# Performance work log

Measured on AMD Instinct MI355X. Metric: run time of the kernel, lower is better.

## Reference

```python
import jax, jax.numpy as jnp
import numpy as np

EMB = 1024
HID = 1024
VOCAB = 32000
SEQ = 128


def _lstm_cell(x, h, c, W_ih, W_hh, b_ih, b_hh):
    # PyTorch gate order: input, forget, cell(g), output
    gates = x @ W_ih.T + b_ih + h @ W_hh.T + b_hh  # [4H]
    i, f, g, o = jnp.split(gates, 4)
    c_new = jax.nn.sigmoid(f) * c + jax.nn.sigmoid(i) * jnp.tanh(g)
    h_new = jax.nn.sigmoid(o) * jnp.tanh(c_new)
    return h_new, c_new


def setup_inputs() -> dict:
    key = jax.random.key(0)
    ks = jax.random.split(key, 12)
    s_emb = 0.02
    s_lstm = 1.0 / np.sqrt(HID)
    return {
        "sentence": jax.random.randint(ks[0], (SEQ,), 0, VOCAB),
        "given_num": 64,
        "emb": jax.random.normal(ks[1], (VOCAB, EMB), jnp.float32) * s_emb,
        "W_ih_lstm": jax.random.normal(ks[2], (4 * HID, EMB), jnp.float32) * s_lstm,
        "W_hh_lstm": jax.random.normal(ks[3], (4 * HID, HID), jnp.float32) * s_lstm,
        "b_ih_lstm": jax.random.normal(ks[4], (4 * HID,), jnp.float32) * s_lstm,
        "b_hh_lstm": jax.random.normal(ks[5], (4 * HID,), jnp.float32) * s_lstm,
        "W_ih_cell": jax.random.normal(ks[6], (4 * HID, EMB), jnp.float32) * s_lstm,
        "W_hh_cell": jax.random.normal(ks[7], (4 * HID, HID), jnp.float32) * s_lstm,
        "b_ih_cell": jax.random.normal(ks[8], (4 * HID,), jnp.float32) * s_lstm,
        "b_hh_cell": jax.random.normal(ks[9], (4 * HID,), jnp.float32) * s_lstm,
        "W_tag": jax.random.normal(ks[10], (VOCAB, HID), jnp.float32) * s_lstm,
        "b_tag": jax.random.normal(ks[11], (VOCAB,), jnp.float32) * s_lstm,
    }


def reference(sentence, given_num, emb, W_ih_lstm, W_hh_lstm, b_ih_lstm, b_hh_lstm,
              W_ih_cell, W_hh_cell, b_ih_cell, b_hh_cell, W_tag, b_tag):
    given_num = int(given_num)  # static (batch-1 rollout, fixed split point)

    # ---- teacher-forced prefix through nn.LSTM (init_hidden -> zeros) ----
    embeds_existing = emb[sentence[:given_num]]  # [g, E]

    def prefix_step(carry, x):
        h, c = carry
        h, c = _lstm_cell(x, h, c, W_ih_lstm, W_hh_lstm, b_ih_lstm, b_hh_lstm)
        return (h, c), h

    h0 = jnp.zeros((HID,), embeds_existing.dtype)
    (h, c), lstm_out = jax.lax.scan(prefix_step, (h0, h0), embeds_existing)
    tag_prefix = lstm_out @ W_tag.T + b_tag  # [g, V]

    # multinomial over softmax(tag) == categorical over logits; only last row's
    # sample is consumed as x_t
    skeys = jax.random.split(jax.random.key(123), SEQ - given_num + 1)
    x_t = jax.random.categorical(skeys[0], tag_prefix[-1])

    def rollout_step(carry, k):
        x_t, h, c = carry
        e = emb[x_t]
        h, c = _lstm_cell(e, h, c, W_ih_cell, W_hh_cell, b_ih_cell, b_hh_cell)
        logits = h @ W_tag.T + b_tag  # [V]
        x_next = jax.random.categorical(k, logits)
        return (x_next, h, c), logits

    _, tag_roll = jax.lax.scan(rollout_step, (x_t, h, c), skeys[1:])  # [S-g, V]

    tag_space = jnp.concatenate([tag_prefix, tag_roll], axis=0)  # [S, V]
    return jax.nn.log_softmax(tag_space, axis=-1)
```

## Files before the change

kernel.cpp:

```cpp
#include <hip/hip_runtime.h>
#include <hip/hip_fp16.h>
#include <cstdint>
#include <cstddef>

#define EMBD 1024
#define HIDD 1024
#define G4   4096
#define VOC  32000
#define SEQL 128
#define GN   64
#define NR   64

#define JAX_PARTITIONABLE 1

__device__ __forceinline__ uint32_t rotl32(uint32_t v, int d) { return (v << d) | (v >> (32 - d)); }

__device__ inline void threefry2x32(uint32_t k0, uint32_t k1, uint32_t x0, uint32_t x1,
                                    uint32_t& o0, uint32_t& o1) {
  uint32_t ks2 = k0 ^ k1 ^ 0x1BD11BDAu;
#define TF_ROUND(r) { x0 += x1; x1 = rotl32(x1, r); x1 ^= x0; }
  x0 += k0;  x1 += k1;
  TF_ROUND(13) TF_ROUND(15) TF_ROUND(26) TF_ROUND(6)
  x0 += k1;  x1 += ks2 + 1u;
  TF_ROUND(17) TF_ROUND(29) TF_ROUND(16) TF_ROUND(24)
  x0 += ks2; x1 += k0 + 2u;
  TF_ROUND(13) TF_ROUND(15) TF_ROUND(26) TF_ROUND(6)
  x0 += k0;  x1 += k1 + 3u;
  TF_ROUND(17) TF_ROUND(29) TF_ROUND(16) TF_ROUND(24)
  x0 += k1;  x1 += ks2 + 4u;
  TF_ROUND(13) TF_ROUND(15) TF_ROUND(26) TF_ROUND(6)
  x0 += ks2; x1 += k0 + 5u;
#undef TF_ROUND
  o0 = x0; o1 = x1;
}

__device__ inline uint32_t rng_bits(uint32_t k0, uint32_t k1, uint32_t idx) {
#if JAX_PARTITIONABLE
  uint32_t h0, h1; threefry2x32(k0, k1, 0u, idx, h0, h1);
  return h0 ^ h1;
#else
  uint32_t h0, h1;
  if (idx < (VOC / 2)) { threefry2x32(k0, k1, idx, idx + (VOC / 2), h0, h1); return h0; }
  else                 { threefry2x32(k0, k1, idx - (VOC / 2), idx, h0, h1); return h1; }
#endif
}

__device__ inline float gumbel_of(uint32_t k0, uint32_t k1, uint32_t idx) {
  uint32_t bits = rng_bits(k0, k1, idx);
  float u = __uint_as_float((bits >> 9) | 0x3f800000u) - 1.0f;
  u = fmaxf(u, 1.17549435e-38f);
  return -logf(-logf(u));
}

__device__ inline unsigned long long packCand(float v, int idx) {
  uint32_t u = __float_as_uint(v);
  u = (u & 0x80000000u) ? ~u : (u | 0x80000000u);
  return ((unsigned long long)u << 32) | (unsigned long long)(0xFFFFFFFFu - (uint32_t)idx);
}

__device__ inline float sigf(float x) { return 1.0f / (1.0f + expf(-x)); }

__device__ __forceinline__ float h2f(unsigned short u) {
  __half_raw hr; hr.x = u;
  return __half2float(__half(hr));
}

__global__ void k_init(uint2* keys, unsigned* counters, float* cbuf, float* h0) {
  int t = threadIdx.x;
#if JAX_PARTITIONABLE
  if (t < NR + 1) {
    uint32_t a, b; threefry2x32(0u, 123u, 0u, (uint32_t)t, a, b);
    keys[t] = make_uint2(a, b);
  }
#else
  __shared__ uint32_t buf[2 * (NR + 1)];
  if (t < NR + 1) {
    uint32_t a, b; threefry2x32(0u, 123u, (uint32_t)t, (uint32_t)(t + NR + 1), a, b);
    buf[t] = a; buf[t + NR + 1] = b;
  }
  __syncthreads();
  if (t < NR + 1) keys[t] = make_uint2(buf[2 * t], buf[2 * t + 1]);
#endif
  for (int i = t; i < 66; i += 256) counters[i] = 0u;
  for (int i = t; i < HIDD; i += 256) { cbuf[i] = 0.0f; h0[i] = 0.0f; }
}

__global__ __launch_bounds__(256) void k_cvt_f16(const float* __restrict__ src,
                                                 unsigned short* __restrict__ dst, int n) {
  int stride = gridDim.x * blockDim.x * 8;
  for (int i = (blockIdx.x * blockDim.x + threadIdx.x) * 8; i < n; i += stride) {
    float4 a = *(const float4*)(src + i);
    float4 b = *(const float4*)(src + i + 4);
    union { unsigned short u[8]; uint4 v; } p;
    __half t;
    t = __float2half(a.x); p.u[0] = __half_raw(t).x;
    t = __float2half(a.y); p.u[1] = __half_raw(t).x;
    t = __float2half(a.z); p.u[2] = __half_raw(t).x;
    t = __float2half(a.w); p.u[3] = __half_raw(t).x;
    t = __float2half(b.x); p.u[4] = __half_raw(t).x;
    t = __float2half(b.y); p.u[5] = __half_raw(t).x;
    t = __float2half(b.z); p.u[6] = __half_raw(t).x;
    t = __float2half(b.w); p.u[7] = __half_raw(t).x;
    *(uint4*)(dst + i) = p.v;
  }
}

__global__ void k_gather(const float* __restrict__ emb, const int* __restrict__ sent,
                         float* __restrict__ X) {
  int m = blockIdx.x;
  int row = sent[m];
  const float4* s = (const float4*)(emb + (size_t)row * EMBD);
  float4* d = (float4*)(X + (size_t)m * EMBD);
  d[threadIdx.x] = s[threadIdx.x];
}

__global__ __launch_bounds__(256) void k_gemm64(const float* __restrict__ A,
                                                const float* __restrict__ B,
                                                const float* __restrict__ bias,
                                                float* __restrict__ C, int ldc) {
  __shared__ float As[64][33];
  __shared__ float Bs[64][33];
  int n0 = blockIdx.x * 64;
  int tn = threadIdx.x & 15, tm = threadIdx.x >> 4;
  float acc[4][4] = {{0.f}};
  for (int k0 = 0; k0 < 1024; k0 += 32) {
    for (int f = threadIdx.x; f < 512; f += 256) {
      int r = f >> 3, c4 = (f & 7) << 2;
      float4 v = *(const float4*)(A + (size_t)r * 1024 + k0 + c4);
      As[r][c4 + 0] = v.x; As[r][c4 + 1] = v.y; As[r][c4 + 2] = v.z; As[r][c4 + 3] = v.w;
      float4 u = *(const float4*)(B + (size_t)(n0 + r) * 1024 + k0 + c4);
      Bs[r][c4 + 0] = u.x; Bs[r][c4 + 1] = u.y; Bs[r][c4 + 2] = u.z; Bs[r][c4 + 3] = u.w;
    }
    __syncthreads();
#pragma unroll
    for (int kk = 0; kk < 32; ++kk) {
      float a0 = As[tm * 4 + 0][kk], a1 = As[tm * 4 + 1][kk];
      float a2 = As[tm * 4 + 2][kk], a3 = As[tm * 4 + 3][kk];
      float b0 = Bs[tn * 4 + 0][kk], b1 = Bs[tn * 4 + 1][kk];
      float b2 = Bs[tn * 4 + 2][kk], b3 = Bs[tn * 4 + 3][kk];
      acc[0][0] += a0 * b0; acc[0][1] += a0 * b1; acc[0][2] += a0 * b2; acc[0][3] += a0 * b3;
      acc[1][0] += a1 * b0; acc[1][1] += a1 * b1; acc[1][2] += a1 * b2; acc[1][3] += a1 * b3;
      acc[2][0] += a2 * b0; acc[2][1] += a2 * b1; acc[2][2] += a2 * b2; acc[2][3] += a2 * b3;
      acc[3][0] += a3 * b0; acc[3][1] += a3 * b1; acc[3][2] += a3 * b2; acc[3][3] += a3 * b3;
    }
    __syncthreads();
  }
#pragma unroll
  for (int i = 0; i < 4; ++i)
#pragma unroll
    for (int j = 0; j < 4; ++j) {
      int m = tm * 4 + i, n = n0 + tn * 4 + j;
      float r = acc[i][j] + (bias ? bias[n] : 0.0f);
      C[(size_t)m * ldc + n] = r;
    }
}

__global__ __launch_bounds__(256) void k_gemm64_f16b(const float* __restrict__ A,
                                                     const unsigned short* __restrict__ B16,
                                                     const float* __restrict__ bias,
                                                     float* __restrict__ C, int ldc) {
  __shared__ float As[64][33];
  __shared__ float Bs[64][33];
  int n0 = blockIdx.x * 64;
  int tn = threadIdx.x & 15, tm = threadIdx.x >> 4;
  float acc[4][4] = {{0.f}};
  for (int k0 = 0; k0 < 1024; k0 += 32) {
    for (int f = threadIdx.x; f < 512; f += 256) {
      int r = f >> 3, c4 = (f & 7) << 2;
      float4 v = *(const float4*)(A + (size_t)r * 1024 + k0 + c4);
      As[r][c4 + 0] = v.x; As[r][c4 + 1] = v.y; As[r][c4 + 2] = v.z; As[r][c4 + 3] = v.w;
    }
    {
      int f = threadIdx.x;
      int r = f >> 2, c8 = (f & 3) << 3;
      union { uint4 v; unsigned short u[8]; } p;
      p.v = *(const uint4*)(B16 + (size_t)(n0 + r) * 1024 + k0 + c8);
#pragma unroll
      for (int j = 0; j < 8; ++j) Bs[r][c8 + j] = h2f(p.u[j]);
    }
    __syncthreads();
#pragma unroll
    for (int kk = 0; kk < 32; ++kk) {
      float a0 = As[tm * 4 + 0][kk], a1 = As[tm * 4 + 1][kk];
      float a2 = As[tm * 4 + 2][kk], a3 = As[tm * 4 + 3][kk];
      float b0 = Bs[tn * 4 + 0][kk], b1 = Bs[tn * 4 + 1][kk];
      float b2 = Bs[tn * 4 + 2][kk], b3 = Bs[tn * 4 + 3][kk];
      acc[0][0] += a0 * b0; acc[0][1] += a0 * b1; acc[0][2] += a0 * b2; acc[0][3] += a0 * b3;
      acc[1][0] += a1 * b0; acc[1][1] += a1 * b1; acc[1][2] += a1 * b2; acc[1][3] += a1 * b3;
      acc[2][0] += a2 * b0; acc[2][1] += a2 * b1; acc[2][2] += a2 * b2; acc[2][3] += a2 * b3;
      acc[3][0] += a3 * b0; acc[3][1] += a3 * b1; acc[3][2] += a3 * b2; acc[3][3] += a3 * b3;
    }
    __syncthreads();
  }
#pragma unroll
  for (int i = 0; i < 4; ++i)
#pragma unroll
    for (int j = 0; j < 4; ++j) {
      int m = tm * 4 + i, n = n0 + tn * 4 + j;
      float r = acc[i][j] + (bias ? bias[n] : 0.0f);
      C[(size_t)m * ldc + n] = r;
    }
}

__global__ __launch_bounds__(256) void k_lstm_pre(const float* __restrict__ Whh,
                                                  const float* __restrict__ bih,
                                                  const float* __restrict__ bhh,
                                                  const float* __restrict__ gx, int t,
                                                  const float* __restrict__ hprev,
                                                  float* __restrict__ cbuf,
                                                  float* __restrict__ hout) {
  __shared__ float gs[4];
  int wave = threadIdx.x >> 6, lane = threadIdx.x & 63;
  int j = blockIdx.x;
  int r = j + (wave << 10);
  const float4* h4 = (const float4*)hprev;
  const float4* w4 = (const float4*)(Whh + (size_t)r * 1024);
  float a = 0.0f;
#pragma unroll
  for (int q = 0; q < 4; ++q) {
    float4 w = w4[lane + (q << 6)];
    float4 h = h4[lane + (q << 6)];
    a += w.x * h.x + w.y * h.y + w.z * h.z + w.w * h.w;
  }
#pragma unroll
  for (int off = 32; off; off >>= 1) a += __shfl_xor(a, off, 64);
  if (lane == 0) gs[wave] = a + gx[(size_t)t * G4 + r] + bih[r] + bhh[r];
  __syncthreads();
  if (threadIdx.x == 0) {
    float gi = gs[0], gf = gs[1], gg = gs[2], go = gs[3];
    float cn = sigf(gf) * cbuf[j] + sigf(gi) * tanhf(gg);
    cbuf[j] = cn;
    hout[j] = sigf(go) * tanhf(cn);
  }
}

__global__ __launch_bounds__(256) void k_lstm_roll(const float* __restrict__ Wih,
                                                   const float* __restrict__ Whh,
                                                   const float* __restrict__ bih,
                                                   const float* __restrict__ bhh,
                                                   const float* __restrict__ emb,
                                                   const int* __restrict__ tok, int t,
                                                   const float* __restrict__ hprev,
                                                   float* __restrict__ cbuf,
                                                   float* __restrict__ hout) {
  __shared__ float gs[4];
  int wave = threadIdx.x >> 6, lane = threadIdx.x & 63;
  int j = blockIdx.x;
  int r = j + (wave << 10);
  int row = tok[t];
  const float4* x4 = (const float4*)(emb + (size_t)row * EMBD);
  const float4* h4 = (const float4*)hprev;
  const float4* wi = (const float4*)(Wih + (size_t)r * 1024);
  const float4* wh = (const float4*)(Whh + (size_t)r * 1024);
  float a = 0.0f;
#pragma unroll
  for (int q = 0; q < 4; ++q) {
    float4 w = wi[lane + (q << 6)];
    float4 x = x4[lane + (q << 6)];
    a += w.x * x.x + w.y * x.y + w.z * x.z + w.w * x.w;
    w = wh[lane + (q << 6)];
    float4 h = h4[lane + (q << 6)];
    a += w.x * h.x + w.y * h.y + w.z * h.z + w.w * h.w;
  }
#pragma unroll
  for (int off = 32; off; off >>= 1) a += __shfl_xor(a, off, 64);
  if (lane == 0) gs[wave] = a + bih[r] + bhh[r];
  __syncthreads();
  if (threadIdx.x == 0) {
    float gi = gs[0], gf = gs[1], gg = gs[2], go = gs[3];
    float cn = sigf(gf) * cbuf[j] + sigf(gi) * tanhf(gg);
    cbuf[j] = cn;
    hout[j] = sigf(go) * tanhf(cn);
  }
}

__global__ __launch_bounds__(256) void k_logits(const float* __restrict__ Wtag,
                                                const float* __restrict__ btag,
                                                const float* __restrict__ h,
                                                float* __restrict__ outrow,
                                                const uint2* __restrict__ keys, int key_idx,
                                                unsigned long long* __restrict__ partials,
                                                unsigned* __restrict__ counter,
                                                int* __restrict__ token_out) {
  __shared__ float sums[64];
  __shared__ unsigned long long red[256];
  __shared__ int amLast;
  int wave = threadIdx.x >> 6, lane = threadIdx.x & 63;
  int r0 = blockIdx.x * 64;
  const float4* h4 = (const float4*)h;
  float4 hv[4];
#pragma unroll
  for (int q = 0; q < 4; ++q) hv[q] = h4[lane + (q << 6)];
  for (int rr = 0; rr < 16; ++rr) {
    int lr = wave * 16 + rr;
    int r = r0 + lr;
    const float4* w4 = (const float4*)(Wtag + (size_t)r * 1024);
    float a = 0.0f;
#pragma unroll
    for (int q = 0; q < 4; ++q) {
      float4 w = w4[lane + (q << 6)];
      a += w.x * hv[q].x + w.y * hv[q].y + w.z * hv[q].z + w.w * hv[q].w;
    }
#pragma unroll
    for (int off = 32; off; off >>= 1) a += __shfl_xor(a, off, 64);
    if (lane == 0) sums[lr] = a;
  }
  __syncthreads();
  unsigned long long best = 0ull;
  if (threadIdx.x < 64) {
    int r = r0 + threadIdx.x;
    float L = sums[threadIdx.x] + btag[r];
    outrow[r] = L;
    uint2 K = keys[key_idx];
    float y = L + gumbel_of(K.x, K.y, (uint32_t)r);
    best = packCand(y, r);
#pragma unroll
    for (int off = 32; off; off >>= 1) {
      unsigned long long o = __shfl_xor(best, off, 64);
      if (o > best) best = o;
    }
    if (threadIdx.x == 0) partials[blockIdx.x] = best;
  }
  __threadfence();
  __syncthreads();
  if (threadIdx.x == 0) amLast = (atomicAdd(counter, 1u) == gridDim.x - 1) ? 1 : 0;
  __syncthreads();
  if (amLast) {
    __threadfence();
    unsigned long long b = 0ull;
    for (int i = threadIdx.x; i < (int)gridDim.x; i += 256) {
      unsigned long long v = *((volatile unsigned long long*)(partials + i));
      if (v > b) b = v;
    }
    red[threadIdx.x] = b;
    __syncthreads();
    for (int s = 128; s; s >>= 1) {
      if (threadIdx.x < s) {
        if (red[threadIdx.x + s] > red[threadIdx.x]) red[threadIdx.x] = red[threadIdx.x + s];
      }
      __syncthreads();
    }
    if (threadIdx.x == 0)
      token_out[0] = (int)(0xFFFFFFFFu - (uint32_t)(red[0] & 0xFFFFFFFFull));
  }
}

__global__ __launch_bounds__(256) void k_logits_f16(const unsigned short* __restrict__ Wt16,
                                                    const float* __restrict__ btag,
                                                    const float* __restrict__ h,
                                                    float* __restrict__ outrow,
                                                    const uint2* __restrict__ keys, int key_idx,
                                                    unsigned long long* __restrict__ partials,
                                                    unsigned* __restrict__ counter,
                                                    int* __restrict__ token_out) {
  __shared__ float sums[64];
  __shared__ unsigned long long red[256];
  __shared__ int amLast;
  int wave = threadIdx.x >> 6, lane = threadIdx.x & 63;
  int r0 = blockIdx.x * 64;
  const float4* h4 = (const float4*)h;
  float4 hq[4];
#pragma unroll
  for (int q = 0; q < 2; ++q) {
    hq[2 * q]     = h4[q * 128 + lane * 2];
    hq[2 * q + 1] = h4[q * 128 + lane * 2 + 1];
  }
  for (int rr = 0; rr < 16; ++rr) {
    int lr = wave * 16 + rr;
    int r = r0 + lr;
    const unsigned short* wrow = Wt16 + (size_t)r * 1024;
    float a = 0.0f;
#pragma unroll
    for (int q = 0; q < 2; ++q) {
      union { uint4 v; unsigned short u[8]; } p;
      p.v = *(const uint4*)(wrow + q * 512 + lane * 8);
      float4 hA = hq[2 * q], hB = hq[2 * q + 1];
      a += h2f(p.u[0]) * hA.x; a += h2f(p.u[1]) * hA.y;
      a += h2f(p.u[2]) * hA.z; a += h2f(p.u[3]) * hA.w;
      a += h2f(p.u[4]) * hB.x; a += h2f(p.u[5]) * hB.y;
      a += h2f(p.u[6]) * hB.z; a += h2f(p.u[7]) * hB.w;
    }
#pragma unroll
    for (int off = 32; off; off >>= 1) a += __shfl_xor(a, off, 64);
    if (lane == 0) sums[lr] = a;
  }
  __syncthreads();
  unsigned long long best = 0ull;
  if (threadIdx.x < 64) {
    int r = r0 + threadIdx.x;
    float L = sums[threadIdx.x] + btag[r];
    outrow[r] = L;
    uint2 K = keys[key_idx];
    float y = L + gumbel_of(K.x, K.y, (uint32_t)r);
    best = packCand(y, r);
#pragma unroll
    for (int off = 32; off; off >>= 1) {
      unsigned long long o = __shfl_xor(best, off, 64);
      if (o > best) best = o;
    }
    if (threadIdx.x == 0) partials[blockIdx.x] = best;
  }
  __threadfence();
  __syncthreads();
  if (threadIdx.x == 0) amLast = (atomicAdd(counter, 1u) == gridDim.x - 1) ? 1 : 0;
  __syncthreads();
  if (amLast) {
    __threadfence();
    unsigned long long b = 0ull;
    for (int i = threadIdx.x; i < (int)gridDim.x; i += 256) {
      unsigned long long v = *((volatile unsigned long long*)(partials + i));
      if (v > b) b = v;
    }
    red[threadIdx.x] = b;
    __syncthreads();
    for (int s = 128; s; s >>= 1) {
      if (threadIdx.x < s) {
        if (red[threadIdx.x + s] > red[threadIdx.x]) red[threadIdx.x] = red[threadIdx.x + s];
      }
      __syncthreads();
    }
    if (threadIdx.x == 0)
      token_out[0] = (int)(0xFFFFFFFFu - (uint32_t)(red[0] & 0xFFFFFFFFull));
  }
}

__global__ __launch_bounds__(256) void k_sample_row(const float* __restrict__ row,
                                                    const uint2* __restrict__ keys, int key_idx,
                                                    unsigned long long* __restrict__ partials,
                                                    unsigned* __restrict__ counter,
                                                    int* __restrict__ token_out) {
  __shared__ unsigned long long red[256];
  __shared__ int amLast;
  int v = blockIdx.x * 256 + threadIdx.x;
  unsigned long long best = 0ull;
  if (v < VOC) {
    uint2 K = keys[key_idx];
    float y = row[v] + gumbel_of(K.x, K.y, (uint32_t)v);
    best = packCand(y, v);
  }
  red[threadIdx.x] = best;
  __syncthreads();
  for (int s = 128; s; s >>= 1) {
    if (threadIdx.x < s) {
      if (red[threadIdx.x + s] > red[threadIdx.x]) red[threadIdx.x] = red[threadIdx.x + s];
    }
    __syncthreads();
  }
  if (threadIdx.x == 0) partials[blockIdx.x] = red[0];
  __threadfence();
  __syncthreads();
  if (threadIdx.x == 0) amLast = (atomicAdd(counter, 1u) == gridDim.x - 1) ? 1 : 0;
  __syncthreads();
  if (amLast) {
    __threadfence();
    unsigned long long b = 0ull;
    for (int i = threadIdx.x; i < (int)gridDim.x; i += 256) {
      unsigned long long val = *((volatile unsigned long long*)(partials + i));
      if (val > b) b = val;
    }
    red[threadIdx.x] = b;
    __syncthreads();
    for (int s = 128; s; s >>= 1) {
      if (threadIdx.x < s) {
        if (red[threadIdx.x + s] > red[threadIdx.x]) red[threadIdx.x] = red[threadIdx.x + s];
      }
      __syncthreads();
    }
    if (threadIdx.x == 0)
      token_out[0] = (int)(0xFFFFFFFFu - (uint32_t)(red[0] & 0xFFFFFFFFull));
  }
}

__global__ __launch_bounds__(256) void k_logsoftmax(float* __restrict__ C) {
  __shared__ float red[256];
  float* row = C + (size_t)blockIdx.x * VOC;
  float m = -INFINITY;
  for (int i = threadIdx.x; i < VOC; i += 256) m = fmaxf(m, row[i]);
  red[threadIdx.x] = m;
  __syncthreads();
  for (int s = 128; s; s >>= 1) {
    if (threadIdx.x < s) red[threadIdx.x] = fmaxf(red[threadIdx.x], red[threadIdx.x + s]);
    __syncthreads();
  }
  m = red[0];
  __syncthreads();
  float sum = 0.0f;
  for (int i = threadIdx.x; i < VOC; i += 256) sum += expf(row[i] - m);
  red[threadIdx.x] = sum;
  __syncthreads();
  for (int s = 128; s; s >>= 1) {
    if (threadIdx.x < s) red[threadIdx.x] += red[threadIdx.x + s];
    __syncthreads();
  }
  float lse = m + logf(red[0]);
  __syncthreads();
  for (int i = threadIdx.x; i < VOC; i += 256) row[i] = row[i] - lse;
}

extern "C" void kernel_launch(void* const* d_in, const int* in_sizes, int n_in,
                              void* d_out, int out_size, void* d_ws, size_t ws_size,
                              hipStream_t stream) {
  (void)in_sizes; (void)n_in; (void)out_size;
  const int*   sent  = (const int*)  d_in[0];
  const float* emb   = (const float*)d_in[2];
  const float* Wih_l = (const float*)d_in[3];
  const float* Whh_l = (const float*)d_in[4];
  const float* bih_l = (const float*)d_in[5];
  const float* bhh_l = (const float*)d_in[6];
  const float* Wih_c = (const float*)d_in[7];
  const float* Whh_c = (const float*)d_in[8];
  const float* bih_c = (const float*)d_in[9];
  const float* bhh_c = (const float*)d_in[10];
  const float* Wtag  = (const float*)d_in[11];
  const float* btag  = (const float*)d_in[12];
  float* out = (float*)d_out;

  char* ws = (char*)d_ws;
  uint2*              keys     = (uint2*)(ws + 0);
  int*                tokens   = (int*)(ws + 1024);
  unsigned*           counters = (unsigned*)(ws + 2048);
  unsigned long long* partials = (unsigned long long*)(ws + 4096);
  float*              cbuf     = (float*)(ws + 12288);
  float*              h0       = (float*)(ws + 16384);
  float*              lstm_out = (float*)(ws + 20480);
  float*              hroll    = (float*)(ws + 20480 + 262144);
  float*              X        = (float*)(ws + 20480 + 2 * 262144);
  float*              gx       = (float*)(ws + 20480 + 3 * 262144);
  const size_t WT16_OFF   = 2u * 1024u * 1024u;
  const size_t WT16_BYTES = (size_t)VOC * 1024u * 2u;
  unsigned short* Wt16 = (unsigned short*)(ws + WT16_OFF);
  bool use16 = (ws_size >= WT16_OFF + WT16_BYTES);

  k_init<<<1, 256, 0, stream>>>(keys, counters, cbuf, h0);
  if (use16)
    k_cvt_f16<<<2048, 256, 0, stream>>>(Wtag, Wt16, VOC * 1024);
  k_gather<<<GN, 256, 0, stream>>>(emb, sent, X);
  k_gemm64<<<G4 / 64, 256, 0, stream>>>(X, Wih_l, nullptr, gx, G4);
  for (int t = 0; t < GN; ++t) {
    const float* hp = t ? (lstm_out + (size_t)(t - 1) * HIDD) : h0;
    k_lstm_pre<<<HIDD, 256, 0, stream>>>(Whh_l, bih_l, bhh_l, gx, t, hp, cbuf,
                                         lstm_out + (size_t)t * HIDD);
  }
  if (use16)
    k_gemm64_f16b<<<VOC / 64, 256, 0, stream>>>(lstm_out, Wt16, btag, out, VOC);
  else
    k_gemm64<<<VOC / 64, 256, 0, stream>>>(lstm_out, Wtag, btag, out, VOC);
  k_sample_row<<<(VOC + 255) / 256, 256, 0, stream>>>(out + (size_t)(GN - 1) * VOC, keys, 0,
                                                      partials, counters + 64, tokens);
  for (int t = 0; t < NR; ++t) {
    const float* hp = t ? (hroll + (size_t)(t - 1) * HIDD) : (lstm_out + (size_t)(GN - 1) * HIDD);
    k_lstm_roll<<<HIDD, 256, 0, stream>>>(Wih_c, Whh_c, bih_c, bhh_c, emb, tokens, t, hp, cbuf,
                                          hroll + (size_t)t * HIDD);
    if (use16)
      k_logits_f16<<<VOC / 64, 256, 0, stream>>>(Wt16, btag, hroll + (size_t)t * HIDD,
                                                 out + (size_t)(GN + t) * VOC, keys, 1 + t,
                                                 partials, counters + t, tokens + t + 1);
    else
      k_logits<<<VOC / 64, 256, 0, stream>>>(Wtag, btag, hroll + (size_t)t * HIDD,
                                             out + (size_t)(GN + t) * VOC, keys, 1 + t,
                                             partials, counters + t, tokens + t + 1);
  }
  k_logsoftmax<<<SEQL, 256, 0, stream>>>(out);
}
```

Before: 4.464 ms.

## Replace per-step LSTM launches with persistent kernels using grid barriers

Result: slower. 5.063 ms (+13.4%).

```diff
diff --git a/kernel.cpp b/kernel.cpp
--- a/kernel.cpp
+++ b/kernel.cpp
@@ -65,7 +65,21 @@
   return __half2float(__half(hr));
 }
 
-__global__ void k_init(uint2* keys, unsigned* counters, float* cbuf, float* h0) {
+__device__ __forceinline__ void gbar(unsigned* bar, unsigned target) {
+  __syncthreads();
+  if (threadIdx.x == 0) {
+    __threadfence();
+    unsigned prev = atomicAdd(bar, 1u);
+    if (prev + 1u < target) {
+      while (*((volatile unsigned*)bar) < target) __builtin_amdgcn_s_sleep(2);
+    }
+    __threadfence();
+  }
+  __syncthreads();
+}
+
+__global__ void k_init(uint2* keys, unsigned* counters, unsigned* bars,
+                       float* cbuf, float* h0) {
   int t = threadIdx.x;
 #if JAX_PARTITIONABLE
   if (t < NR + 1) {
@@ -82,6 +96,7 @@
   if (t < NR + 1) keys[t] = make_uint2(buf[2 * t], buf[2 * t + 1]);
 #endif
   for (int i = t; i < 66; i += 256) counters[i] = 0u;
+  for (int i = t; i < 1024; i += 256) bars[i] = 0u;
   for (int i = t; i < HIDD; i += 256) { cbuf[i] = 0.0f; h0[i] = 0.0f; }
 }
 
@@ -200,6 +215,167 @@
       float r = acc[i][j] + (bias ? bias[n] : 0.0f);
       C[(size_t)m * ldc + n] = r;
     }
+}
+
+__global__ __launch_bounds__(512) void k_prefix_persist(
+    const float* __restrict__ Whh, const float* __restrict__ bih,
+    const float* __restrict__ bhh, const float* __restrict__ gx,
+    const float* __restrict__ h0, float* __restrict__ lstm_out,
+    float* __restrict__ cbuf_out, unsigned* __restrict__ bars) {
+  int b = blockIdx.x;
+  int wave = threadIdx.x >> 6, lane = threadIdx.x & 63;
+  int j0 = b * 4;
+  __shared__ float gs[16];
+  __shared__ float cl[4];
+  if (threadIdx.x < 4) cl[threadIdx.x] = 0.0f;
+  __syncthreads();
+  for (int t = 0; t < GN; ++t) {
+    const float* hprev = t ? (lstm_out + (size_t)(t - 1) * HIDD) : h0;
+    const float4* h4 = (const float4*)hprev;
+    float4 hv[4];
+#pragma unroll
+    for (int q = 0; q < 4; ++q) hv[q] = h4[lane + (q << 6)];
+#pragma unroll
+    for (int rr = 0; rr < 2; ++rr) {
+      int rl = wave + (rr << 3);
+      int gate = rl >> 2, jj = rl & 3;
+      int r = (j0 + jj) + (gate << 10);
+      const float4* w4 = (const float4*)(Whh + (size_t)r * 1024);
+      float a = 0.0f;
+#pragma unroll
+      for (int q = 0; q < 4; ++q) {
+        float4 w = w4[lane + (q << 6)];
+        a += w.x * hv[q].x + w.y * hv[q].y + w.z * hv[q].z + w.w * hv[q].w;
+      }
+#pragma unroll
+      for (int off = 32; off; off >>= 1) a += __shfl_xor(a, off, 64);
+      if (lane == 0) gs[rl] = a + gx[(size_t)t * G4 + r] + bih[r] + bhh[r];
+    }
+    __syncthreads();
+    if (threadIdx.x < 4) {
+      int jj = threadIdx.x;
+      float gi = gs[jj], gf = gs[4 + jj], gg = gs[8 + jj], go = gs[12 + jj];
+      float cn = sigf(gf) * cl[jj] + sigf(gi) * tanhf(gg);
+      cl[jj] = cn;
+      lstm_out[(size_t)t * HIDD + j0 + jj] = sigf(go) * tanhf(cn);
+      if (t == GN - 1) cbuf_out[j0 + jj] = cn;
+    }
+    gbar(bars + t, gridDim.x);
+  }
+}
+
+__global__ __launch_bounds__(512) void k_roll_persist(
+    const float* __restrict__ Wih, const float* __restrict__ Whh,
+    const float* __restrict__ bih, const float* __restrict__ bhh,
+    const float* __restrict__ emb, const unsigned short* __restrict__ Wt16,
+    const float* __restrict__ btag, const float* __restrict__ cbuf_in,
+    const float* __restrict__ h_last, float* __restrict__ hbuf,
+    float* __restrict__ out, const uint2* __restrict__ keys,
+    int* __restrict__ tokens, unsigned long long* __restrict__ partials,
+    unsigned* __restrict__ bars) {
+  int b = blockIdx.x;
+  int wave = threadIdx.x >> 6, lane = threadIdx.x & 63;
+  int j0 = b * 4;
+  __shared__ float gs[16];
+  __shared__ float cl[4];
+  __shared__ unsigned long long wmax[8];
+  __shared__ unsigned long long pr[256];
+  if (threadIdx.x < 4) cl[threadIdx.x] = cbuf_in[j0 + threadIdx.x];
+  int token = tokens[0];
+  __syncthreads();
+  for (int t = 0; t < NR; ++t) {
+    const float* hprev = t ? (hbuf + (size_t)(t - 1) * HIDD) : h_last;
+    const float4* h4 = (const float4*)hprev;
+    const float4* x4 = (const float4*)(emb + (size_t)token * EMBD);
+    float4 hv[4], xv[4];
+#pragma unroll
+    for (int q = 0; q < 4; ++q) { hv[q] = h4[lane + (q << 6)]; xv[q] = x4[lane + (q << 6)]; }
+#pragma unroll
+    for (int rr = 0; rr < 2; ++rr) {
+      int rl = wave + (rr << 3);
+      int gate = rl >> 2, jj = rl & 3;
+      int r = (j0 + jj) + (gate << 10);
+      const float4* wi = (const float4*)(Wih + (size_t)r * 1024);
+      const float4* wh = (const float4*)(Whh + (size_t)r * 1024);
+      float a = 0.0f;
+#pragma unroll
+      for (int q = 0; q < 4; ++q) {
+        float4 w = wi[lane + (q << 6)];
+        a += w.x * xv[q].x + w.y * xv[q].y + w.z * xv[q].z + w.w * xv[q].w;
+        w = wh[lane + (q << 6)];
+        a += w.x * hv[q].x + w.y * hv[q].y + w.z * hv[q].z + w.w * hv[q].w;
+      }
+#pragma unroll
+      for (int off = 32; off; off >>= 1) a += __shfl_xor(a, off, 64);
+      if (lane == 0) gs[rl] = a + bih[r] + bhh[r];
+    }
+    __syncthreads();
+    if (threadIdx.x < 4) {
+      int jj = threadIdx.x;
+      float gi = gs[jj], gf = gs[4 + jj], gg = gs[8 + jj], go = gs[12 + jj];
+      float cn = sigf(gf) * cl[jj] + sigf(gi) * tanhf(gg);
+      cl[jj] = cn;
+      hbuf[(size_t)t * HIDD + j0 + jj] = sigf(go) * tanhf(cn);
+    }
+    gbar(bars + 64 + 2 * t, gridDim.x);
+    const float* hh = hbuf + (size_t)t * HIDD;
+    const float4* hh4 = (const float4*)hh;
+    float4 hq[4];
+#pragma unroll
+    for (int q = 0; q < 2; ++q) {
+      hq[2 * q]     = hh4[q * 128 + lane * 2];
+      hq[2 * q + 1] = hh4[q * 128 + lane * 2 + 1];
+    }
+    uint2 K = keys[1 + t];
+    float* outrow = out + (size_t)(GN + t) * VOC;
+    unsigned long long best = 0ull;
+    for (int rl = wave; rl < 125; rl += 8) {
+      int r = b * 125 + rl;
+      const unsigned short* wrow = Wt16 + (size_t)r * 1024;
+      float a = 0.0f;
+#pragma unroll
+      for (int q = 0; q < 2; ++q) {
+        union { uint4 v; unsigned short u[8]; } p;
+        p.v = *(const uint4*)(wrow + q * 512 + lane * 8);
+        float4 hA = hq[2 * q], hB = hq[2 * q + 1];
+        a += h2f(p.u[0]) * hA.x; a += h2f(p.u[1]) * hA.y;
+        a += h2f(p.u[2]) * hA.z; a += h2f(p.u[3]) * hA.w;
+        a += h2f(p.u[4]) * hB.x; a += h2f(p.u[5]) * hB.y;
+        a += h2f(p.u[6]) * hB.z; a += h2f(p.u[7]) * hB.w;
+      }
+#pragma unroll
+      for (int off = 32; off; off >>= 1) a += __shfl_xor(a, off, 64);
+      if (lane == 0) {
+        float L = a + btag[r];
+        outrow[r] = L;
+        float y = L + gumbel_of(K.x, K.y, (uint32_t)r);
+        unsigned long long cand = packCand(y, r);
+        if (cand > best) best = cand;
+      }
+    }
+    if (lane == 0) wmax[wave] = best;
+    __syncthreads();
+    if (threadIdx.x == 0) {
+      unsigned long long bb = wmax[0];
+#pragma unroll
+      for (int w = 1; w < 8; ++w) if (wmax[w] > bb) bb = wmax[w];
+      partials[b] = bb;
+    }
+    gbar(bars + 64 + 2 * t + 1, gridDim.x);
+    if (t + 1 < NR) {
+      if (threadIdx.x < 256) pr[threadIdx.x] = *((volatile unsigned long long*)(partials + threadIdx.x));
+      __syncthreads();
+      for (int s = 128; s; s >>= 1) {
+        if (threadIdx.x < s) {
+          if (pr[threadIdx.x + s] > pr[threadIdx.x]) pr[threadIdx.x] = pr[threadIdx.x + s];
+        }
+        __syncthreads();
+      }
+      token = (int)(0xFFFFFFFFu - (uint32_t)(pr[0] & 0xFFFFFFFFull));
+      if (b == 0 && threadIdx.x == 0) tokens[t + 1] = token;
+      __syncthreads();
+    }
+  }
 }
 
 __global__ __launch_bounds__(256) void k_lstm_pre(const float* __restrict__ Whh,
@@ -345,85 +521,6 @@
   }
 }
 
-__global__ __launch_bounds__(256) void k_logits_f16(const unsigned short* __restrict__ Wt16,
-                                                    const float* __restrict__ btag,
-                                                    const float* __restrict__ h,
-                                                    float* __restrict__ outrow,
-                                                    const uint2* __restrict__ keys, int key_idx,
-                                                    unsigned long long* __restrict__ partials,
-                                                    unsigned* __restrict__ counter,
-                                                    int* __restrict__ token_out) {
-  __shared__ float sums[64];
-  __shared__ unsigned long long red[256];
-  __shared__ int amLast;
-  int wave = threadIdx.x >> 6, lane = threadIdx.x & 63;
-  int r0 = blockIdx.x * 64;
-  const float4* h4 = (const float4*)h;
-  float4 hq[4];
-#pragma unroll
-  for (int q = 0; q < 2; ++q) {
-    hq[2 * q]     = h4[q * 128 + lane * 2];
-    hq[2 * q + 1] = h4[q * 128 + lane * 2 + 1];
-  }
-  for (int rr = 0; rr < 16; ++rr) {
-    int lr = wave * 16 + rr;
-    int r = r0 + lr;
-    const unsigned short* wrow = Wt16 + (size_t)r * 1024;
-    float a = 0.0f;
-#pragma unroll
-    for (int q = 0; q < 2; ++q) {
-      union { uint4 v; unsigned short u[8]; } p;
-      p.v = *(const uint4*)(wrow + q * 512 + lane * 8);
-      float4 hA = hq[2 * q], hB = hq[2 * q + 1];
-      a += h2f(p.u[0]) * hA.x; a += h2f(p.u[1]) * hA.y;
-      a += h2f(p.u[2]) * hA.z; a += h2f(p.u[3]) * hA.w;
-      a += h2f(p.u[4]) * hB.x; a += h2f(p.u[5]) * hB.y;
-      a += h2f(p.u[6]) * hB.z; a += h2f(p.u[7]) * hB.w;
-    }
-#pragma unroll
-    for (int off = 32; off; off >>= 1) a += __shfl_xor(a, off, 64);
-    if (lane == 0) sums[lr] = a;
-  }
-  __syncthreads();
-  unsigned long long best = 0ull;
-  if (threadIdx.x < 64) {
-    int r = r0 + threadIdx.x;
-    float L = sums[threadIdx.x] + btag[r];
-    outrow[r] = L;
-    uint2 K = keys[key_idx];
-    float y = L + gumbel_of(K.x, K.y, (uint32_t)r);
-    best = packCand(y, r);
-#pragma unroll
-    for (int off = 32; off; off >>= 1) {
-      unsigned long long o = __shfl_xor(best, off, 64);
-      if (o > best) best = o;
-    }
-    if (threadIdx.x == 0) partials[blockIdx.x] = best;
-  }
-  __threadfence();
-  __syncthreads();
-  if (threadIdx.x == 0) amLast = (atomicAdd(counter, 1u) == gridDim.x - 1) ? 1 : 0;
-  __syncthreads();
-  if (amLast) {
-    __threadfence();
-    unsigned long long b = 0ull;
-    for (int i = threadIdx.x; i < (int)gridDim.x; i += 256) {
-      unsigned long long v = *((volatile unsigned long long*)(partials + i));
-      if (v > b) b = v;
-    }
-    red[threadIdx.x] = b;
-    __syncthreads();
-    for (int s = 128; s; s >>= 1) {
-      if (threadIdx.x < s) {
-        if (red[threadIdx.x + s] > red[threadIdx.x]) red[threadIdx.x] = red[threadIdx.x + s];
-      }
-      __syncthreads();
-    }
-    if (threadIdx.x == 0)
-      token_out[0] = (int)(0xFFFFFFFFu - (uint32_t)(red[0] & 0xFFFFFFFFull));
-  }
-}
-
 __global__ __launch_bounds__(256) void k_sample_row(const float* __restrict__ row,
                                                     const uint2* __restrict__ keys, int key_idx,
                                                     unsigned long long* __restrict__ partials,
@@ -519,46 +616,51 @@
   uint2*              keys     = (uint2*)(ws + 0);
   int*                tokens   = (int*)(ws + 1024);
   unsigned*           counters = (unsigned*)(ws + 2048);
-  unsigned long long* partials = (unsigned long long*)(ws + 4096);
-  float*              cbuf     = (float*)(ws + 12288);
-  float*              h0       = (float*)(ws + 16384);
-  float*              lstm_out = (float*)(ws + 20480);
-  float*              hroll    = (float*)(ws + 20480 + 262144);
-  float*              X        = (float*)(ws + 20480 + 2 * 262144);
-  float*              gx       = (float*)(ws + 20480 + 3 * 262144);
+  unsigned*           bars     = (unsigned*)(ws + 4096);
+  unsigned long long* partials = (unsigned long long*)(ws + 8192);
+  float*              cbuf     = (float*)(ws + 16384);
+  float*              h0       = (float*)(ws + 20480);
+  float*              lstm_out = (float*)(ws + 24576);
+  float*              hroll    = (float*)(ws + 24576 + 262144);
+  float*              X        = (float*)(ws + 24576 + 2 * 262144);
+  float*              gx       = (float*)(ws + 24576 + 3 * 262144);
   const size_t WT16_OFF   = 2u * 1024u * 1024u;
   const size_t WT16_BYTES = (size_t)VOC * 1024u * 2u;
   unsigned short* Wt16 = (unsigned short*)(ws + WT16_OFF);
   bool use16 = (ws_size >= WT16_OFF + WT16_BYTES);
 
-  k_init<<<1, 256, 0, stream>>>(keys, counters, cbuf, h0);
+  k_init<<<1, 256, 0, stream>>>(keys, counters, bars, cbuf, h0);
   if (use16)
     k_cvt_f16<<<2048, 256, 0, stream>>>(Wtag, Wt16, VOC * 1024);
   k_gather<<<GN, 256, 0, stream>>>(emb, sent, X);
   k_gemm64<<<G4 / 64, 256, 0, stream>>>(X, Wih_l, nullptr, gx, G4);
-  for (int t = 0; t < GN; ++t) {
-    const float* hp = t ? (lstm_out + (size_t)(t - 1) * HIDD) : h0;
-    k_lstm_pre<<<HIDD, 256, 0, stream>>>(Whh_l, bih_l, bhh_l, gx, t, hp, cbuf,
-                                         lstm_out + (size_t)t * HIDD);
-  }
-  if (use16)
+
+  if (use16) {
+    k_prefix_persist<<<256, 512, 0, stream>>>(Whh_l, bih_l, bhh_l, gx, h0,
+                                              lstm_out, cbuf, bars);
     k_gemm64_f16b<<<VOC / 64, 256, 0, stream>>>(lstm_out, Wt16, btag, out, VOC);
-  else
+    k_sample_row<<<(VOC + 255) / 256, 256, 0, stream>>>(out + (size_t)(GN - 1) * VOC, keys, 0,
+                                                        partials, counters + 64, tokens);
+    k_roll_persist<<<256, 512, 0, stream>>>(Wih_c, Whh_c, bih_c, bhh_c, emb, Wt16, btag,
+                                            cbuf, lstm_out + (size_t)(GN - 1) * HIDD,
+                                            hroll, out, keys, tokens, partials, bars);
+  } else {
+    for (int t = 0; t < GN; ++t) {
+      const float* hp = t ? (lstm_out + (size_t)(t - 1) * HIDD) : h0;
+      k_lstm_pre<<<HIDD, 256, 0, stream>>>(Whh_l, bih_l, bhh_l, gx, t, hp, cbuf,
+                                           lstm_out + (size_t)t * HIDD);
+    }
     k_gemm64<<<VOC / 64, 256, 0, stream>>>(lstm_out, Wtag, btag, out, VOC);
-  k_sample_row<<<(VOC + 255) / 256, 256, 0, stream>>>(out + (size_t)(GN - 1) * VOC, keys, 0,
-                                                      partials, counters + 64, tokens);
-  for (int t = 0; t < NR; ++t) {
-    const float* hp = t ? (hroll + (size_t)(t - 1) * HIDD) : (lstm_out + (size_t)(GN - 1) * HIDD);
-    k_lstm_roll<<<HIDD, 256, 0, stream>>>(Wih_c, Whh_c, bih_c, bhh_c, emb, tokens, t, hp, cbuf,
-                                          hroll + (size_t)t * HIDD);
-    if (use16)
-      k_logits_f16<<<VOC / 64, 256, 0, stream>>>(Wt16, btag, hroll + (size_t)t * HIDD,
-                                                 out + (size_t)(GN + t) * VOC, keys, 1 + t,
-                                                 partials, counters + t, tokens + t + 1);
-    else
+    k_sample_row<<<(VOC + 255) / 256, 256, 0, stream>>>(out + (size_t)(GN - 1) * VOC, keys, 0,
+                                                        partials, counters + 64, tokens);
+    for (int t = 0; t < NR; ++t) {
+      const float* hp = t ? (hroll + (size_t)(t - 1) * HIDD) : (lstm_out + (size_t)(GN - 1) * HIDD);
+      k_lstm_roll<<<HIDD, 256, 0, stream>>>(Wih_c, Whh_c, bih_c, bhh_c, emb, tokens, t, hp, cbuf,
+                                            hroll + (size_t)t * HIDD);
       k_logits<<<VOC / 64, 256, 0, stream>>>(Wtag, btag, hroll + (size_t)t * HIDD,
                                              out + (size_t)(GN + t) * VOC, keys, 1 + t,
                                              partials, counters + t, tokens + t + 1);
+    }
   }
   k_logsoftmax<<<SEQL, 256, 0, stream>>>(out);
 }
```
